# Kernel optimization log

Hardware: AMD Instinct MI355X
Metric: run time of the kernel (lower is better)

The kernel has to match this reference:

```python
import jax, jax.numpy as jnp
import numpy as np

N_ATOMS = 32768
N_GRAPHS = 256
PER_GRAPH = 128
HIDDEN = 128
FILTERS = 128
NUM_GAUSS = 50
CUTOFF = 5.0
NUM_LAYERS = 3
OUT_CH = 1
BOX = 14.1
SLOPE = 0.015


def _lrelu(x):
    return jnp.where(x > 0, x, SLOPE * x)


def setup_inputs() -> dict:
    rng = np.random.default_rng(0)
    batch = np.repeat(np.arange(N_GRAPHS), PER_GRAPH).astype(np.int64)
    pos_np = rng.uniform(0.0, BOX, size=(N_ATOMS, 3)).astype(np.float32)
    # radius graph, built per-graph exactly like compute_radius_graph
    # (with global index offset so edges reference global node ids)
    edges = []
    for b in range(N_GRAPHS):
        pb = pos_np[b * PER_GRAPH:(b + 1) * PER_GRAPH]
        d = np.linalg.norm(pb[:, None, :] - pb[None, :, :], axis=-1)
        src, dst = np.where((d <= CUTOFF) & (d > 0))
        edges.append(np.stack([src, dst], axis=0) + b * PER_GRAPH)
    edge_index = np.concatenate(edges, axis=1).astype(np.int64)
    z = rng.integers(0, 100, size=(N_ATOMS,)).astype(np.int64)

    key = jax.random.key(0)
    ks = jax.random.split(key, 12)

    def xavier(k, shape):
        fan_in, fan_out = shape[-2], shape[-1]
        s = float(np.sqrt(6.0 / (fan_in + fan_out)))
        return jax.random.uniform(k, shape, jnp.float32, -s, s)

    L = NUM_LAYERS
    params = dict(
        emb=jax.random.normal(ks[0], (100, HIDDEN), jnp.float32),
        w_lin=xavier(ks[1], (L, HIDDEN, FILTERS)),
        mlp_w1=xavier(ks[2], (L, NUM_GAUSS, FILTERS)), mlp_b1=jnp.zeros((L, FILTERS), jnp.float32),
        mlp_w2=xavier(ks[3], (L, FILTERS, FILTERS)), mlp_b2=jnp.zeros((L, FILTERS), jnp.float32),
        mlp_w3=xavier(ks[4], (L, FILTERS, FILTERS)), mlp_b3=jnp.zeros((L, FILTERS), jnp.float32),
        lout_w=xavier(ks[5], (L, FILTERS, FILTERS)), lout_b=jnp.zeros((L, FILTERS), jnp.float32),
        v_w1=xavier(ks[6], (L, FILTERS, HIDDEN)), v_b1=jnp.zeros((L, HIDDEN), jnp.float32),
        v_w2=xavier(ks[7], (L, HIDDEN, HIDDEN)), v_b2=jnp.zeros((L, HIDDEN), jnp.float32),
        u_w1=xavier(ks[8], (HIDDEN, HIDDEN // 2)), u_b1=jnp.zeros((HIDDEN // 2,), jnp.float32),
        u_w2=xavier(ks[9], (HIDDEN // 2, OUT_CH)), u_b2=jnp.zeros((OUT_CH,), jnp.float32),
    )
    return dict(z=jnp.asarray(z), pos=jnp.asarray(pos_np), batch=jnp.asarray(batch),
                edge_index=jnp.asarray(edge_index), **params)


def reference(z, pos, batch, edge_index, emb, w_lin,
              mlp_w1, mlp_b1, mlp_w2, mlp_b2, mlp_w3, mlp_b3,
              lout_w, lout_b, v_w1, v_b1, v_w2, v_b2,
              u_w1, u_b1, u_w2, u_b2):
    row, col = edge_index[0], edge_index[1]          # row = j (source), col = i (target)
    dist = jnp.linalg.norm(pos[row] - pos[col], axis=-1)        # [E]
    offset = jnp.linspace(0.0, CUTOFF, NUM_GAUSS)
    coeff = -0.5 / (offset[1] - offset[0]) ** 2
    dist_emb = jnp.exp(coeff * (dist[:, None] - offset[None, :]) ** 2)   # [E, G]
    C = 0.5 * (jnp.cos(dist * jnp.pi / CUTOFF) + 1.0)                    # [E]

    v = emb[z]                                                           # [N, H]
    for l in range(NUM_LAYERS):
        # UpdateE: filter MLP on distance embedding, cosine cutoff envelope
        h = _lrelu(dist_emb @ mlp_w1[l] + mlp_b1[l])
        h = _lrelu(h @ mlp_w2[l] + mlp_b2[l])
        W = (h @ mlp_w3[l] + mlp_b3[l]) * C[:, None]                     # [E, F]
        e = (v @ w_lin[l])[row] * W                                      # gather + modulate
        e = (e @ lout_w[l] + lout_b[l]) + e                              # residual edge lin
        # UpdateV: scatter-add into target nodes, then 2-layer MLP residual
        agg = jax.ops.segment_sum(e, col, num_segments=N_ATOMS)         # [N, F]
        v = v + (_lrelu(agg @ v_w1[l] + v_b1[l]) @ v_w2[l] + v_b2[l])

    # UpdateU: node MLP then per-graph mean pooling
    u = _lrelu(v @ u_w1 + u_b1) @ u_w2 + u_b2                            # [N, out]
    sums = jax.ops.segment_sum(u, batch, num_segments=N_GRAPHS)
    cnt = jax.ops.segment_sum(jnp.ones((u.shape[0],), u.dtype), batch, num_segments=N_GRAPHS)
    return jnp.where(cnt[:, None] > 0, sums / jnp.maximum(cnt, 1.0)[:, None], 0.0)
```

## Files before the change

### kernel.cpp

```cpp
#include <hip/hip_runtime.h>

typedef float f4 __attribute__((ext_vector_type(4)));
typedef float f2 __attribute__((ext_vector_type(2)));
typedef float f32x4 __attribute__((ext_vector_type(4)));
typedef short bf16x8 __attribute__((ext_vector_type(8)));
typedef short sh4 __attribute__((ext_vector_type(4)));
typedef unsigned short us4 __attribute__((ext_vector_type(4)));

#define G_TAB 8192
#define SWZ(row, b) ((b) ^ (((row) & 7) << 4))

__device__ __forceinline__ float lrelu(float x) { return x > 0.f ? x : 0.015f * x; }

__device__ __forceinline__ short f2bf(float x) {
  union { float f; unsigned u; } v; v.f = x;
  unsigned r = v.u + 0x7fff + ((v.u >> 16) & 1);
  return (short)(r >> 16);
}
__device__ __forceinline__ float bf2f(short h) {
  union { float f; unsigned u; } v; v.u = ((unsigned)(unsigned short)h) << 16;
  return v.f;
}
__device__ __forceinline__ float bf2fu(unsigned short h) {
  union { float f; unsigned u; } v; v.u = ((unsigned)h) << 16;
  return v.f;
}

__device__ __forceinline__ void st_pair(short* Hi, short* Lo, int row, int k, f4 x) {
  sh4 hi, lo;
  #pragma unroll
  for (int c = 0; c < 4; c++) { hi[c] = f2bf(x[c]); lo[c] = f2bf(x[c] - bf2f(hi[c])); }
  int b = row * 256 + SWZ(row, (k >> 3) * 16) + (k & 7) * 2;
  *(sh4*)((char*)Hi + b) = hi;
  *(sh4*)((char*)Lo + b) = lo;
}
__device__ __forceinline__ void st_pair1(short* Hi, short* Lo, int row, int k, float x) {
  short hi = f2bf(x), lo = f2bf(x - bf2f(hi));
  int b = row * 256 + SWZ(row, (k >> 3) * 16) + (k & 7) * 2;
  *(short*)((char*)Hi + b) = hi;
  *(short*)((char*)Lo + b) = lo;
}

template<int NFC, int CH>
__device__ __forceinline__ void mm16(const short* Ahi, const short* Alo,
    const short* __restrict__ BhT, const short* __restrict__ BlT,
    int w, int l, f32x4* acc) {
  int lr = l & 15, lk = l >> 4;
  #pragma unroll
  for (int fc = 0; fc < NFC; fc++) acc[fc] = (f32x4)0.f;
  #pragma unroll
  for (int ch = 0; ch < CH; ch++) {
    int arow = w * 16 + lr;
    int ab = arow * 256 + SWZ(arow, ch * 64 + lk * 16);
    bf16x8 ah = *(const bf16x8*)((const char*)Ahi + ab);
    bf16x8 al = *(const bf16x8*)((const char*)Alo + ab);
    #pragma unroll
    for (int fc = 0; fc < NFC; fc++) {
      int bcol = fc * 16 + lr;
      int bb = bcol * 256 + SWZ(bcol, ch * 64 + lk * 16);
      bf16x8 bh = *(const bf16x8*)((const char*)BhT + bb);
      bf16x8 bl = *(const bf16x8*)((const char*)BlT + bb);
      acc[fc] = __builtin_amdgcn_mfma_f32_16x16x32_bf16(ah, bh, acc[fc], 0, 0, 0);
      acc[fc] = __builtin_amdgcn_mfma_f32_16x16x32_bf16(al, bh, acc[fc], 0, 0, 0);
      acc[fc] = __builtin_amdgcn_mfma_f32_16x16x32_bf16(ah, bl, acc[fc], 0, 0, 0);
    }
  }
}


__global__ __launch_bounds__(256) void gather_emb(const int* __restrict__ z,
    const float* __restrict__ emb, float* __restrict__ v, int nf4) {
  int i = blockIdx.x * 256 + threadIdx.x;
  if (i >= nf4) return;
  int a = i >> 5, s = i & 31;
  ((f4*)v)[i] = ((const f4*)emb)[z[a] * 32 + s];
}

__global__ __launch_bounds__(256) void edge_geom(const int* __restrict__ ei,
    const float* __restrict__ pos, float* __restrict__ edc, int E) {
  int e = blockIdx.x * 256 + threadIdx.x;
  if (e >= E) return;
  int r = ei[e], c = ei[E + e];
  float dx = pos[3*r] - pos[3*c];
  float dy = pos[3*r+1] - pos[3*c+1];
  float dz = pos[3*r+2] - pos[3*c+2];
  float d = sqrtf(dx*dx + dy*dy + dz*dz);
  edc[2*e] = d;
  edc[2*e+1] = 0.5f * (cosf(d * 0.6283185307179586f) + 1.0f);
}

__global__ __launch_bounds__(256) void make_starts(const int* __restrict__ row,
    int* __restrict__ starts, int E, int N) {
  int i = blockIdx.x * 256 + threadIdx.x;
  if (i > N) return;
  int lo = 0, hi = E;
  while (lo < hi) { int mid = (lo + hi) >> 1; if (row[mid] < i) lo = mid + 1; else hi = mid; }
  starts[i] = lo;
}

__global__ __launch_bounds__(256) void convert_wt(const float* __restrict__ w_lin,
    const float* __restrict__ vw2, const float* __restrict__ uw1,
    const float* __restrict__ mw1, const float* __restrict__ mw2,
    const float* __restrict__ mw3, const float* __restrict__ vw1,
    short* __restrict__ dhi, short* __restrict__ dlo) {
  int y = blockIdx.y;
  int i = blockIdx.x * 256 + threadIdx.x;
  int k = i >> 7, j = i & 127;
  int slot; float x;
  if (y < 3)       { slot = y;     x = w_lin[(size_t)y*16384 + k*128 + j]; }
  else if (y < 6)  { slot = 3 + y; x = vw2[(size_t)(y-3)*16384 + k*128 + j]; }
  else if (y == 6) { slot = 9;     x = (j < 64) ? uw1[k*64 + j] : 0.f; }
  else if (y < 10) { slot = 3 + y; x = mw2[(size_t)(y-7)*16384 + k*128 + j]; }
  else if (y < 13) { slot = 3 + y; x = mw3[(size_t)(y-10)*16384 + k*128 + j]; }
  else if (y < 16) { slot = 3 + y; x = (k < 50) ? mw1[(size_t)(y-13)*6400 + k*128 + j] : 0.f; }
  else             { slot = 3 + y; x = vw1[(size_t)(y-16)*16384 + k*128 + j]; }
  short hi = f2bf(x);
  int ob = j * 256 + (((k >> 3) * 16) ^ ((j & 7) << 4)) + (k & 7) * 2;
  char* bh = (char*)dhi + (size_t)slot * 32768;
  char* bl = (char*)dlo + (size_t)slot * 32768;
  *(short*)(bh + ob) = hi;
  *(short*)(bl + ob) = f2bf(x - bf2f(hi));
}

__global__ __launch_bounds__(128) void make_c1(const float* __restrict__ lball,
    const float* __restrict__ w1all, float* __restrict__ c1all) {
  int l = blockIdx.y;
  const float* lb = lball + (size_t)l * 128;
  const float* w1 = w1all + (size_t)l * 16384;
  int j = threadIdx.x;
  float s = 0.f;
  for (int k = 0; k < 128; k++) s += lb[k] * w1[k * 128 + j];
  c1all[l * 128 + j] = s;
}

__global__ __launch_bounds__(512) void prep_M(const float* __restrict__ loutw,
    short* __restrict__ whiT, short* __restrict__ wloT) {
  __shared__ __align__(16) short Ahi[16384];
  __shared__ __align__(16) short Alo[16384];
  int tid = threadIdx.x;
  int lay = blockIdx.x;
  int w = tid >> 6, l = tid & 63;
  int lr = l & 15, lk = l >> 4;
  int arow = w * 16 + (l >> 2), sub = l & 3;
  const f4* src = (const f4*)(loutw + (size_t)lay*16384 + (size_t)arow*128 + sub*32);
  #pragma unroll
  for (int q = 0; q < 8; q++) {
    f4 x = src[q];
    int kb = sub * 32 + q * 4;
    #pragma unroll
    for (int cc = 0; cc < 4; cc++) if (arow == kb + cc) x[cc] += 1.0f;
    st_pair(Ahi, Alo, arow, kb, x);
  }
  __syncthreads();
  f32x4 acc[8];
  mm16<8,4>(Ahi, Alo, whiT + (size_t)(19+lay)*16384, wloT + (size_t)(19+lay)*16384, w, l, acc);
  char* bh = (char*)whiT + (size_t)(3+lay) * 32768;
  char* bl = (char*)wloT + (size_t)(3+lay) * 32768;
  #pragma unroll
  for (int r = 0; r < 4; r++)
    #pragma unroll
    for (int fc = 0; fc < 8; fc++) {
      int row = w*16 + lk*4 + r, col = fc*16 + lr;
      float val = acc[fc][r];
      short hi = f2bf(val);
      int ob = col * 256 + (((row >> 3) * 16) ^ ((col & 7) << 4)) + (row & 7) * 2;
      *(short*)(bh + ob) = hi;
      *(short*)(bl + ob) = f2bf(val - bf2f(hi));
    }
}

__global__ __launch_bounds__(512) void table_mfma(
    const short* __restrict__ whiT, const short* __restrict__ wloT,
    const float* __restrict__ mb1, const float* __restrict__ mb2,
    const float* __restrict__ mb3, unsigned short* __restrict__ tables) {
  __shared__ __align__(16) short Ahi[16384];
  __shared__ __align__(16) short Alo[16384];
  __shared__ __align__(16) short Bhi[16384];
  __shared__ __align__(16) short Blo[16384];
  int tid = threadIdx.x;
  int lay = blockIdx.y;
  int p0 = blockIdx.x * 128;
  int w = tid >> 6, l = tid & 63;
  int lr = l & 15, lk = l >> 4;
  int prow = w * 16 + (l >> 2), sub = l & 3;
  const float delta = 5.0f / (G_TAB - 1);
  {
    float d = (p0 + prow) * delta;
    #pragma unroll
    for (int q = 0; q < 4; q++) {
      f4 x;
      #pragma unroll
      for (int cc = 0; cc < 4; cc++) {
        int k = sub * 16 + q * 4 + cc;
        float t = d - k * (5.0f / 49.0f);
        x[cc] = (k < 50) ? expf(-48.02f * t * t) : 0.f;
      }
      st_pair(Ahi, Alo, prow, sub * 16 + q * 4, x);
    }
  }
  __syncthreads();
  f32x4 acc[8];
  mm16<8,2>(Ahi, Alo, whiT + (size_t)(16+lay)*16384, wloT + (size_t)(16+lay)*16384, w, l, acc);
  #pragma unroll
  for (int r = 0; r < 4; r++)
    #pragma unroll
    for (int fc = 0; fc < 8; fc++)
      st_pair1(Bhi, Blo, w*16 + lk*4 + r, fc*16 + lr,
               lrelu(acc[fc][r] + mb1[lay*128 + fc*16 + lr]));
  __syncthreads();
  mm16<8,4>(Bhi, Blo, whiT + (size_t)(10+lay)*16384, wloT + (size_t)(10+lay)*16384, w, l, acc);
  #pragma unroll
  for (int r = 0; r < 4; r++)
    #pragma unroll
    for (int fc = 0; fc < 8; fc++)
      st_pair1(Ahi, Alo, w*16 + lk*4 + r, fc*16 + lr,
               lrelu(acc[fc][r] + mb2[lay*128 + fc*16 + lr]));
  __syncthreads();
  mm16<8,4>(Ahi, Alo, whiT + (size_t)(13+lay)*16384, wloT + (size_t)(13+lay)*16384, w, l, acc);
  unsigned short* tb = tables + (size_t)lay * G_TAB * 128;
  #pragma unroll
  for (int r = 0; r < 4; r++)
    #pragma unroll
    for (int fc = 0; fc < 8; fc++)
      tb[(size_t)(p0 + w*16 + lk*4 + r) * 128 + fc*16 + lr] =
          (unsigned short)f2bf(acc[fc][r] + mb3[lay*128 + fc*16 + lr]);
}


template<int ACT, int ACC, int BIAS, int ABF, int OBF>
__global__ __launch_bounds__(256) void gemm128b(
    const void* __restrict__ Ain, const short* __restrict__ BhS,
    const short* __restrict__ BlS, const float* __restrict__ bias,
    const float* __restrict__ bias2, const float* __restrict__ rs,
    void* __restrict__ outv) {
  __shared__ __align__(16) short Bhi[16384];
  int tid = threadIdx.x;
  int p = blockIdx.x;
  size_t row0 = (size_t)(((p & 7) << 5) + (p >> 3)) * 128;
  #pragma unroll
  for (int s = 0; s < 8; s++)
    ((bf16x8*)Bhi)[tid + 256*s] = ((const bf16x8*)BhS)[tid + 256*s];
  __syncthreads();
  int w = tid >> 6, l = tid & 63, lr = l & 15, lk = l >> 4;
  const char* BlB = (const char*)BlS;
  #pragma unroll
  for (int half = 0; half < 2; half++) {
    int rbase = half * 64 + w * 16;
    bf16x8 ah[4], al[4];
    if (ABF) {
      const short* ap0 = (const short*)Ain + (row0 + rbase + lr) * 128;
      #pragma unroll
      for (int ch = 0; ch < 4; ch++)
        ah[ch] = *(const bf16x8*)(ap0 + ch*32 + lk*8);
    } else {
      const float* ap0 = (const float*)Ain + (row0 + rbase + lr) * 128;
      #pragma unroll
      for (int ch = 0; ch < 4; ch++) {
        const f4* ap = (const f4*)(ap0 + ch*32 + lk*8);
        f4 x0 = ap[0], x1 = ap[1];
        #pragma unroll
        for (int c = 0; c < 4; c++) {
          short h0 = f2bf(x0[c]);
          ah[ch][c] = h0; al[ch][c] = f2bf(x0[c] - bf2f(h0));
          short h1 = f2bf(x1[c]);
          ah[ch][c+4] = h1; al[ch][c+4] = f2bf(x1[c] - bf2f(h1));
        }
      }
    }
    f32x4 acc[8];
    #pragma unroll
    for (int fc = 0; fc < 8; fc++) acc[fc] = (f32x4)0.f;
    #pragma unroll
    for (int ch = 0; ch < 4; ch++)
      #pragma unroll
      for (int fc = 0; fc < 8; fc++) {
        int bcol = fc*16 + lr;
        int bb = bcol*256 + SWZ(bcol, ch*64 + lk*16);
        bf16x8 bh = *(const bf16x8*)((const char*)Bhi + bb);
        bf16x8 bl = *(const bf16x8*)(BlB + bb);
        acc[fc] = __builtin_amdgcn_mfma_f32_16x16x32_bf16(ah[ch], bh, acc[fc], 0, 0, 0);
        if (!ABF)
          acc[fc] = __builtin_amdgcn_mfma_f32_16x16x32_bf16(al[ch], bh, acc[fc], 0, 0, 0);
        acc[fc] = __builtin_amdgcn_mfma_f32_16x16x32_bf16(ah[ch], bl, acc[fc], 0, 0, 0);
      }
    #pragma unroll
    for (int r = 0; r < 4; r++) {
      size_t grow = row0 + rbase + lk*4 + r;
      float rsv = (BIAS == 3) ? rs[grow] : 0.f;
      #pragma unroll
      for (int fc = 0; fc < 8; fc++) {
        int col = fc*16 + lr;
        float val = acc[fc][r];
        if (BIAS == 1) val += bias[col];
        if (BIAS == 3) val += rsv * bias[col] + bias2[col];
        if (ACT) val = lrelu(val);
        if (OBF) {
          ((short*)outv)[grow * 128 + col] = f2bf(val);
        } else {
          float* op = (float*)outv + grow * 128 + col;
          if (ACC) val += *op;
          *op = val;
        }
      }
    }
  }
}

__global__ __launch_bounds__(256) void edge_gather(
    const int* __restrict__ ei, const int* __restrict__ starts,
    const float* __restrict__ edc, const unsigned short* __restrict__ vlinb,
    const unsigned short* __restrict__ tb, float* __restrict__ S,
    float* __restrict__ deg, int E, int N) {
  int tid = threadIdx.x;
  int lane = tid & 63, grp = tid >> 6;
  int half = lane >> 5, fl = lane & 31;
  int p = blockIdx.x;
  int o = ((p & 7) << 10) + (p >> 3);
  int a = o * 4 + grp;
  if (a >= N) return;
  int s = starts[a], ee = starts[a + 1];
  int mid = s + ((ee - s + 1) >> 1);
  int e0 = half ? mid : s;
  int e1 = half ? ee : mid;
  int j0 = fl * 4;
  const float sc = (float)(G_TAB - 1) / 5.0f;
  f4 acc = (f4)0.f;
  int e = e0;
  for (; e + 3 < e1; e += 4) {
    int cc[4]; f2 dd[4];
    #pragma unroll
    for (int q = 0; q < 4; q++) { cc[q] = ei[E + e + q]; dd[q] = *(const f2*)&edc[2*(e+q)]; }
    us4 vl[4], t[4];
    #pragma unroll
    for (int q = 0; q < 4; q++) {
      int i0 = (int)(dd[q][0] * sc + 0.5f);
      if (i0 > G_TAB - 1) i0 = G_TAB - 1;
      t[q] = *(const us4*)&tb[(size_t)i0 * 128 + j0];
      vl[q] = *(const us4*)&vlinb[(size_t)cc[q] * 128 + j0];
    }
    #pragma unroll
    for (int q = 0; q < 4; q++) {
      f4 T, V;
      #pragma unroll
      for (int c4 = 0; c4 < 4; c4++) { T[c4] = bf2fu(t[q][c4]); V[c4] = bf2fu(vl[q][c4]); }
      acc += V * (T * dd[q][1]);
    }
  }
  for (; e < e1; e++) {
    int c0 = ei[E + e];
    f2 dc0 = *(const f2*)&edc[2 * e];
    int i0 = (int)(dc0[0] * sc + 0.5f);
    if (i0 > G_TAB - 1) i0 = G_TAB - 1;
    us4 t = *(const us4*)&tb[(size_t)i0 * 128 + j0];
    us4 vl = *(const us4*)&vlinb[(size_t)c0 * 128 + j0];
    f4 T, V;
    #pragma unroll
    for (int c4 = 0; c4 < 4; c4++) { T[c4] = bf2fu(t[c4]); V[c4] = bf2fu(vl[c4]); }
    acc += V * (T * dc0[1]);
  }
  #pragma unroll
  for (int c4 = 0; c4 < 4; c4++) acc[c4] += __shfl_xor(acc[c4], 32);
  if (half == 0) *(f4*)&S[(size_t)a * 128 + j0] = acc;
  if (lane == 0) deg[a] = (float)(ee - s);
}

__global__ __launch_bounds__(256) void readout_b(const float* __restrict__ v,
    const short* __restrict__ Bh9, const short* __restrict__ Bl9,
    const float* __restrict__ ub1, const float* __restrict__ uw2,
    float* __restrict__ y) {
  __shared__ __align__(16) short Bh[8192];
  int tid = threadIdx.x;
  int p = blockIdx.x;
  size_t row0 = (size_t)(((p & 7) << 5) + (p >> 3)) * 128;
  #pragma unroll
  for (int s = 0; s < 4; s++)
    ((bf16x8*)Bh)[tid + 256*s] = ((const bf16x8*)Bh9)[tid + 256*s];
  __syncthreads();
  int w = tid >> 6, l = tid & 63, lr = l & 15, lk = l >> 4;
  const char* BlB = (const char*)Bl9;
  #pragma unroll
  for (int half = 0; half < 2; half++) {
    int rbase = half * 64 + w * 16;
    const float* ap0 = v + (row0 + rbase + lr) * 128;
    bf16x8 ah[4], al[4];
    #pragma unroll
    for (int ch = 0; ch < 4; ch++) {
      const f4* ap = (const f4*)(ap0 + ch*32 + lk*8);
      f4 x0 = ap[0], x1 = ap[1];
      #pragma unroll
      for (int c = 0; c < 4; c++) {
        short h0 = f2bf(x0[c]);
        ah[ch][c] = h0; al[ch][c] = f2bf(x0[c] - bf2f(h0));
        short h1 = f2bf(x1[c]);
        ah[ch][c+4] = h1; al[ch][c+4] = f2bf(x1[c] - bf2f(h1));
      }
    }
    f32x4 acc[4];
    #pragma unroll
    for (int fc = 0; fc < 4; fc++) acc[fc] = (f32x4)0.f;
    #pragma unroll
    for (int ch = 0; ch < 4; ch++)
      #pragma unroll
      for (int fc = 0; fc < 4; fc++) {
        int bcol = fc*16 + lr;
        int bb = bcol*256 + SWZ(bcol, ch*64 + lk*16);
        bf16x8 bh = *(const bf16x8*)((const char*)Bh + bb);
        bf16x8 bl = *(const bf16x8*)(BlB + bb);
        acc[fc] = __builtin_amdgcn_mfma_f32_16x16x32_bf16(ah[ch], bh, acc[fc], 0, 0, 0);
        acc[fc] = __builtin_amdgcn_mfma_f32_16x16x32_bf16(al[ch], bh, acc[fc], 0, 0, 0);
        acc[fc] = __builtin_amdgcn_mfma_f32_16x16x32_bf16(ah[ch], bl, acc[fc], 0, 0, 0);
      }
    #pragma unroll
    for (int r = 0; r < 4; r++) {
      float sv = 0.f;
      #pragma unroll
      for (int fc = 0; fc < 4; fc++) {
        int col = fc*16 + lr;
        sv += lrelu(acc[fc][r] + ub1[col]) * uw2[col];
      }
      sv += __shfl_xor(sv, 1); sv += __shfl_xor(sv, 2);
      sv += __shfl_xor(sv, 4); sv += __shfl_xor(sv, 8);
      if (lr == 0) y[row0 + rbase + lk*4 + r] = sv;
    }
  }
}

__global__ __launch_bounds__(256) void graph_mean(const float* __restrict__ y,
    const float* __restrict__ ub2, float* __restrict__ out) {
  __shared__ float red[256];
  int tid = threadIdx.x;
  red[tid] = y[blockIdx.x * 256 + tid];
  __syncthreads();
  for (int s = 64; s > 0; s >>= 1) {
    if ((tid & 127) < s) red[tid] += red[tid + s];
    __syncthreads();
  }
  if ((tid & 127) == 0)
    out[blockIdx.x * 2 + (tid >> 7)] = red[tid] * (1.0f / 128.0f) + ub2[0];
}

extern "C" void kernel_launch(void* const* d_in, const int* in_sizes, int n_in,
                              void* d_out, int out_size, void* d_ws, size_t ws_size,
                              hipStream_t stream) {
  const int*   z     = (const int*)d_in[0];
  const float* pos   = (const float*)d_in[1];
  const int*   ei    = (const int*)d_in[3];
  const float* emb   = (const float*)d_in[4];
  const float* w_lin = (const float*)d_in[5];
  const float* mw1   = (const float*)d_in[6];
  const float* mb1   = (const float*)d_in[7];
  const float* mw2   = (const float*)d_in[8];
  const float* mb2   = (const float*)d_in[9];
  const float* mw3   = (const float*)d_in[10];
  const float* mb3   = (const float*)d_in[11];
  const float* loutw = (const float*)d_in[12];
  const float* loutb = (const float*)d_in[13];
  const float* vw1   = (const float*)d_in[14];
  const float* vb1   = (const float*)d_in[15];
  const float* vw2   = (const float*)d_in[16];
  const float* vb2   = (const float*)d_in[17];
  const float* uw1   = (const float*)d_in[18];
  const float* ub1   = (const float*)d_in[19];
  const float* uw2   = (const float*)d_in[20];
  const float* ub2   = (const float*)d_in[21];
  int N = in_sizes[0];
  int E = in_sizes[3] / 2;
  float* out = (float*)d_out;

  size_t off = 0;
  auto alloc = [&](size_t bytes) -> void* {
    void* p = (char*)d_ws + off;
    off += (bytes + 255) & ~(size_t)255;
    return p;
  };
  float* v      = (float*)alloc((size_t)N * 128 * 4);
  unsigned short* vlinb = (unsigned short*)alloc((size_t)N * 128 * 2);
  float* Sbuf   = (float*)alloc((size_t)N * 128 * 4);
  short* t16    = (short*)alloc((size_t)N * 128 * 2);
  unsigned short* tables = (unsigned short*)alloc((size_t)3 * G_TAB * 128 * 2);
  short* whiT   = (short*)alloc((size_t)22 * 16384 * 2);
  short* wloT   = (short*)alloc((size_t)22 * 16384 * 2);
  float* c1s    = (float*)alloc(3 * 128 * 4);
  float* deg    = (float*)alloc((size_t)N * 4);
  float* edc    = (float*)alloc((size_t)E * 8);
  int*   starts = (int*)alloc((size_t)(N + 1) * 4);
  float* y      = (float*)alloc((size_t)N * 4);

  gather_emb<<<(N * 32 + 255) / 256, 256, 0, stream>>>(z, emb, v, N * 32);
  edge_geom<<<(E + 255) / 256, 256, 0, stream>>>(ei, pos, edc, E);
  make_starts<<<(N + 256) / 256, 256, 0, stream>>>(ei, starts, E, N);
  convert_wt<<<dim3(64, 19), 256, 0, stream>>>(w_lin, vw2, uw1, mw1, mw2, mw3, vw1,
                                               whiT, wloT);
  prep_M<<<3, 512, 0, stream>>>(loutw, whiT, wloT);
  make_c1<<<dim3(1, 3), 128, 0, stream>>>(loutb, vw1, c1s);
  table_mfma<<<dim3(G_TAB / 128, 3), 512, 0, stream>>>(whiT, wloT, mb1, mb2, mb3, tables);

  for (int l = 0; l < 3; l++) {
    gemm128b<0, 0, 0, 0, 1><<<N / 128, 256, 0, stream>>>(
        v, whiT + (size_t)l * 16384, wloT + (size_t)l * 16384,
        nullptr, nullptr, nullptr, vlinb);
    edge_gather<<<N / 4, 256, 0, stream>>>(ei, starts, edc, vlinb,
                                           tables + (size_t)l * G_TAB * 128,
                                           Sbuf, deg, E, N);
    gemm128b<1, 0, 3, 0, 1><<<N / 128, 256, 0, stream>>>(
        Sbuf, whiT + (size_t)(3 + l) * 16384, wloT + (size_t)(3 + l) * 16384,
        c1s + (size_t)l * 128, vb1 + (size_t)l * 128, deg, t16);
    gemm128b<0, 1, 1, 1, 0><<<N / 128, 256, 0, stream>>>(
        t16, whiT + (size_t)(6 + l) * 16384, wloT + (size_t)(6 + l) * 16384,
        vb2 + (size_t)l * 128, nullptr, nullptr, v);
  }
  readout_b<<<N / 128, 256, 0, stream>>>(v, whiT + (size_t)9 * 16384,
                                         wloT + (size_t)9 * 16384, ub1, uw2, y);
  graph_mean<<<N / 256, 256, 0, stream>>>(y, ub2, out);
}
```

Baseline: 311.7 us.

## Fuse per-graph v@W_lin GEMM with edge gather via LDS-resident node features

Each block now owns one 128-atom graph. It computes v@W_lin for that graph with MFMA and keeps the bf16 result in LDS, then gathers edge messages from LDS instead of a global vlinb buffer. This drops one kernel launch per layer and the global write and read of vlinb, relying on edges staying inside their own graph. Only 256 blocks with 4 waves each now do the gather work, which cuts parallelism compared with the previous 8192-block gather kernel. The intermediate t16 buffer also changes from bf16 to fp32, which raises memory traffic but keeps precision.

```diff
diff --git a/kernel.cpp b/kernel.cpp
--- a/kernel.cpp
+++ b/kernel.cpp
@@ -9,6 +9,7 @@
 
 #define G_TAB 8192
 #define SWZ(row, b) ((b) ^ (((row) & 7) << 4))
+#define VP 132
 
 __device__ __forceinline__ float lrelu(float x) { return x > 0.f ? x : 0.015f * x; }
 
@@ -227,6 +228,119 @@
 }
 
 
+__global__ __launch_bounds__(256) void vlin_gather(
+    const float* __restrict__ v, const short* __restrict__ BhS,
+    const short* __restrict__ BlS, const int* __restrict__ ei,
+    const int* __restrict__ starts, const float* __restrict__ edc,
+    const unsigned short* __restrict__ tb, float* __restrict__ S,
+    float* __restrict__ deg, int E) {
+  __shared__ __align__(16) short Bhi[16384];
+  __shared__ __align__(16) unsigned short vlds[128 * VP];
+  int tid = threadIdx.x;
+  int p = blockIdx.x;
+  int g = ((p & 7) << 5) + (p >> 3);
+  size_t row0 = (size_t)g * 128;
+  #pragma unroll
+  for (int s = 0; s < 8; s++)
+    ((bf16x8*)Bhi)[tid + 256*s] = ((const bf16x8*)BhS)[tid + 256*s];
+  __syncthreads();
+  int w = tid >> 6, l = tid & 63, lr = l & 15, lk = l >> 4;
+  const char* BlB = (const char*)BlS;
+  #pragma unroll
+  for (int half = 0; half < 2; half++) {
+    int rbase = half * 64 + w * 16;
+    const float* ap0 = v + (row0 + rbase + lr) * 128;
+    bf16x8 ah[4], al[4];
+    #pragma unroll
+    for (int ch = 0; ch < 4; ch++) {
+      const f4* ap = (const f4*)(ap0 + ch*32 + lk*8);
+      f4 x0 = ap[0], x1 = ap[1];
+      #pragma unroll
+      for (int c = 0; c < 4; c++) {
+        short h0 = f2bf(x0[c]);
+        ah[ch][c] = h0; al[ch][c] = f2bf(x0[c] - bf2f(h0));
+        short h1 = f2bf(x1[c]);
+        ah[ch][c+4] = h1; al[ch][c+4] = f2bf(x1[c] - bf2f(h1));
+      }
+    }
+    f32x4 acc[8];
+    #pragma unroll
+    for (int fc = 0; fc < 8; fc++) acc[fc] = (f32x4)0.f;
+    #pragma unroll
+    for (int ch = 0; ch < 4; ch++)
+      #pragma unroll
+      for (int fc = 0; fc < 8; fc++) {
+        int bcol = fc*16 + lr;
+        int bb = bcol*256 + SWZ(bcol, ch*64 + lk*16);
+        bf16x8 bh = *(const bf16x8*)((const char*)Bhi + bb);
+        bf16x8 bl = *(const bf16x8*)(BlB + bb);
+        acc[fc] = __builtin_amdgcn_mfma_f32_16x16x32_bf16(ah[ch], bh, acc[fc], 0, 0, 0);
+        acc[fc] = __builtin_amdgcn_mfma_f32_16x16x32_bf16(al[ch], bh, acc[fc], 0, 0, 0);
+        acc[fc] = __builtin_amdgcn_mfma_f32_16x16x32_bf16(ah[ch], bl, acc[fc], 0, 0, 0);
+      }
+    #pragma unroll
+    for (int r = 0; r < 4; r++) {
+      int row = rbase + lk*4 + r;
+      #pragma unroll
+      for (int fc = 0; fc < 8; fc++)
+        vlds[row * VP + fc*16 + lr] = (unsigned short)f2bf(acc[fc][r]);
+    }
+  }
+  __syncthreads();
+  int half2 = l >> 5, fl = l & 31;
+  int j0 = fl * 4;
+  const float sc = (float)(G_TAB - 1) / 5.0f;
+  for (int ai = 0; ai < 32; ai++) {
+    int arow = w * 32 + ai;
+    int a = (int)row0 + arow;
+    int s0 = starts[a], ee = starts[a + 1];
+    int mid = s0 + ((ee - s0 + 1) >> 1);
+    int e0 = half2 ? mid : s0;
+    int e1 = half2 ? ee : mid;
+    f4 acc = (f4)0.f;
+    int e = e0;
+    for (; e + 3 < e1; e += 4) {
+      int cc[4]; f2 dd[4];
+      #pragma unroll
+      for (int q = 0; q < 4; q++) {
+        cc[q] = ei[E + e + q] - (int)row0;
+        dd[q] = *(const f2*)&edc[2*(e+q)];
+      }
+      us4 vl[4], t[4];
+      #pragma unroll
+      for (int q = 0; q < 4; q++) {
+        int i0 = (int)(dd[q][0] * sc + 0.5f);
+        if (i0 > G_TAB - 1) i0 = G_TAB - 1;
+        t[q] = *(const us4*)&tb[(size_t)i0 * 128 + j0];
+        vl[q] = *(const us4*)&vlds[cc[q] * VP + j0];
+      }
+      #pragma unroll
+      for (int q = 0; q < 4; q++) {
+        f4 T, V;
+        #pragma unroll
+        for (int c4 = 0; c4 < 4; c4++) { T[c4] = bf2fu(t[q][c4]); V[c4] = bf2fu(vl[q][c4]); }
+        acc += V * (T * dd[q][1]);
+      }
+    }
+    for (; e < e1; e++) {
+      int c0 = ei[E + e] - (int)row0;
+      f2 dc0 = *(const f2*)&edc[2 * e];
+      int i0 = (int)(dc0[0] * sc + 0.5f);
+      if (i0 > G_TAB - 1) i0 = G_TAB - 1;
+      us4 t = *(const us4*)&tb[(size_t)i0 * 128 + j0];
+      us4 vl = *(const us4*)&vlds[c0 * VP + j0];
+      f4 T, V;
+      #pragma unroll
+      for (int c4 = 0; c4 < 4; c4++) { T[c4] = bf2fu(t[c4]); V[c4] = bf2fu(vl[c4]); }
+      acc += V * (T * dc0[1]);
+    }
+    #pragma unroll
+    for (int c4 = 0; c4 < 4; c4++) acc[c4] += __shfl_xor(acc[c4], 32);
+    if (half2 == 0) *(f4*)&S[(size_t)a * 128 + j0] = acc;
+    if (l == 0) deg[a] = (float)(ee - s0);
+  }
+}
+
 template<int ACT, int ACC, int BIAS, int ABF, int OBF>
 __global__ __launch_bounds__(256) void gemm128b(
     const void* __restrict__ Ain, const short* __restrict__ BhS,
@@ -304,64 +418,6 @@
       }
     }
   }
-}
-
-__global__ __launch_bounds__(256) void edge_gather(
-    const int* __restrict__ ei, const int* __restrict__ starts,
-    const float* __restrict__ edc, const unsigned short* __restrict__ vlinb,
-    const unsigned short* __restrict__ tb, float* __restrict__ S,
-    float* __restrict__ deg, int E, int N) {
-  int tid = threadIdx.x;
-  int lane = tid & 63, grp = tid >> 6;
-  int half = lane >> 5, fl = lane & 31;
-  int p = blockIdx.x;
-  int o = ((p & 7) << 10) + (p >> 3);
-  int a = o * 4 + grp;
-  if (a >= N) return;
-  int s = starts[a], ee = starts[a + 1];
-  int mid = s + ((ee - s + 1) >> 1);
-  int e0 = half ? mid : s;
-  int e1 = half ? ee : mid;
-  int j0 = fl * 4;
-  const float sc = (float)(G_TAB - 1) / 5.0f;
-  f4 acc = (f4)0.f;
-  int e = e0;
-  for (; e + 3 < e1; e += 4) {
-    int cc[4]; f2 dd[4];
-    #pragma unroll
-    for (int q = 0; q < 4; q++) { cc[q] = ei[E + e + q]; dd[q] = *(const f2*)&edc[2*(e+q)]; }
-    us4 vl[4], t[4];
-    #pragma unroll
-    for (int q = 0; q < 4; q++) {
-      int i0 = (int)(dd[q][0] * sc + 0.5f);
-      if (i0 > G_TAB - 1) i0 = G_TAB - 1;
-      t[q] = *(const us4*)&tb[(size_t)i0 * 128 + j0];
-      vl[q] = *(const us4*)&vlinb[(size_t)cc[q] * 128 + j0];
-    }
-    #pragma unroll
-    for (int q = 0; q < 4; q++) {
-      f4 T, V;
-      #pragma unroll
-      for (int c4 = 0; c4 < 4; c4++) { T[c4] = bf2fu(t[q][c4]); V[c4] = bf2fu(vl[q][c4]); }
-      acc += V * (T * dd[q][1]);
-    }
-  }
-  for (; e < e1; e++) {
-    int c0 = ei[E + e];
-    f2 dc0 = *(const f2*)&edc[2 * e];
-    int i0 = (int)(dc0[0] * sc + 0.5f);
-    if (i0 > G_TAB - 1) i0 = G_TAB - 1;
-    us4 t = *(const us4*)&tb[(size_t)i0 * 128 + j0];
-    us4 vl = *(const us4*)&vlinb[(size_t)c0 * 128 + j0];
-    f4 T, V;
-    #pragma unroll
-    for (int c4 = 0; c4 < 4; c4++) { T[c4] = bf2fu(t[c4]); V[c4] = bf2fu(vl[c4]); }
-    acc += V * (T * dc0[1]);
-  }
-  #pragma unroll
-  for (int c4 = 0; c4 < 4; c4++) acc[c4] += __shfl_xor(acc[c4], 32);
-  if (half == 0) *(f4*)&S[(size_t)a * 128 + j0] = acc;
-  if (lane == 0) deg[a] = (float)(ee - s);
 }
 
 __global__ __launch_bounds__(256) void readout_b(const float* __restrict__ v,
@@ -474,9 +530,8 @@
     return p;
   };
   float* v      = (float*)alloc((size_t)N * 128 * 4);
-  unsigned short* vlinb = (unsigned short*)alloc((size_t)N * 128 * 2);
   float* Sbuf   = (float*)alloc((size_t)N * 128 * 4);
-  short* t16    = (short*)alloc((size_t)N * 128 * 2);
+  float* bufC   = (float*)alloc((size_t)N * 128 * 4);
   unsigned short* tables = (unsigned short*)alloc((size_t)3 * G_TAB * 128 * 2);
   short* whiT   = (short*)alloc((size_t)22 * 16384 * 2);
   short* wloT   = (short*)alloc((size_t)22 * 16384 * 2);
@@ -496,17 +551,14 @@
   table_mfma<<<dim3(G_TAB / 128, 3), 512, 0, stream>>>(whiT, wloT, mb1, mb2, mb3, tables);
 
   for (int l = 0; l < 3; l++) {
-    gemm128b<0, 0, 0, 0, 1><<<N / 128, 256, 0, stream>>>(
+    vlin_gather<<<N / 128, 256, 0, stream>>>(
         v, whiT + (size_t)l * 16384, wloT + (size_t)l * 16384,
-        nullptr, nullptr, nullptr, vlinb);
-    edge_gather<<<N / 4, 256, 0, stream>>>(ei, starts, edc, vlinb,
-                                           tables + (size_t)l * G_TAB * 128,
-                                           Sbuf, deg, E, N);
-    gemm128b<1, 0, 3, 0, 1><<<N / 128, 256, 0, stream>>>(
+        ei, starts, edc, tables + (size_t)l * G_TAB * 128, Sbuf, deg, E);
+    gemm128b<1, 0, 3, 0, 0><<<N / 128, 256, 0, stream>>>(
         Sbuf, whiT + (size_t)(3 + l) * 16384, wloT + (size_t)(3 + l) * 16384,
-        c1s + (size_t)l * 128, vb1 + (size_t)l * 128, deg, t16);
-    gemm128b<0, 1, 1, 1, 0><<<N / 128, 256, 0, stream>>>(
-        t16, whiT + (size_t)(6 + l) * 16384, wloT + (size_t)(6 + l) * 16384,
+        c1s + (size_t)l * 128, vb1 + (size_t)l * 128, deg, bufC);
+    gemm128b<0, 1, 1, 0, 0><<<N / 128, 256, 0, stream>>>(
+        bufC, whiT + (size_t)(6 + l) * 16384, wloT + (size_t)(6 + l) * 16384,
         vb2 + (size_t)l * 128, nullptr, nullptr, v);
   }
   readout_b<<<N / 128, 256, 0, stream>>>(v, whiT + (size_t)9 * 16384,
```

Result: slower. 378.1 us (+21.3%).
